# Optimization experiments

Measured on AMD Instinct MI355X. Metric: run time of the kernel, lower is better.

## Reference

```python
import jax, jax.numpy as jnp
import numpy as np

B, S, D, H, HD = 2, 4096, 1024, 16, 64   # batch, seq, hidden, heads, head_dim
BLOCK, W = 64, 8                          # block size, local window in blocks (512 tokens)
ROPE_BASE = 10000.0


def _rope_tables(seq_len, dim, dtype):
    inv_freq = 1.0 / (ROPE_BASE ** (jnp.arange(0, dim, 2, dtype=jnp.float32) / dim))
    t = jnp.arange(seq_len, dtype=jnp.float32)
    freqs = jnp.einsum('i,j->ij', t, inv_freq)          # [S, dim/2]
    emb = jnp.concatenate([freqs, freqs], axis=-1)       # [S, dim]
    return jnp.cos(emb).astype(dtype), jnp.sin(emb).astype(dtype)


def _rotate_half(x):
    x1, x2 = x[..., : x.shape[-1] // 2], x[..., x.shape[-1] // 2:]
    return jnp.concatenate([-x2, x1], axis=-1)


def _apply_rope(q, k, position_ids):
    # q, k: [B, H, S, HD]; position_ids: [B, S]
    cos_t, sin_t = _rope_tables(S, HD, q.dtype)
    cos = cos_t[position_ids][:, None, :, :]             # [B, 1, S, HD]
    sin = sin_t[position_ids][:, None, :, :]
    q_emb = q * cos + _rotate_half(q) * sin
    k_emb = k * cos + _rotate_half(k) * sin
    return q_emb, k_emb


def _block_sparse_attention(q, k, v):
    # Causal block-sparse (sliding window of W blocks), DeepSpeed-style layout.
    # q, k, v: [B, H, S, HD]
    nb = S // BLOCK
    scale = 1.0 / jnp.sqrt(jnp.asarray(HD, q.dtype))
    qb = q.reshape(B, H, nb, BLOCK, HD)
    kb = k.reshape(B, H, nb, BLOCK, HD)
    vb = v.reshape(B, H, nb, BLOCK, HD)
    # block-column indices attended by each block-row: i-W+1 .. i
    idx = jnp.arange(nb)[:, None] - jnp.arange(W - 1, -1, -1)[None, :]   # [nb, W]
    valid = idx >= 0
    idxc = jnp.clip(idx, 0, nb - 1)
    kg = kb[:, :, idxc]                                   # [B, H, nb, W, BLOCK, HD]
    vg = vb[:, :, idxc]
    scores = jnp.einsum('bhnqd,bhnwkd->bhnqwk', qb, kg) * scale  # [B,H,nb,BLOCK,W,BLOCK]
    # absolute positions for causal mask within the window
    qpos = (jnp.arange(nb) * BLOCK)[:, None, None, None] + jnp.arange(BLOCK)[None, :, None, None]  # [nb,BLOCK,1,1]
    kpos = (idxc * BLOCK)[:, None, :, None] + jnp.arange(BLOCK)[None, None, None, :]               # [nb,1,W,BLOCK]
    mask = (kpos <= qpos) & valid[:, None, :, None]       # [nb, BLOCK, W, BLOCK]
    neg = jnp.asarray(-1e9, scores.dtype)
    scores = jnp.where(mask[None, None], scores, neg)
    scores = scores.reshape(B, H, nb, BLOCK, W * BLOCK)
    probs = jax.nn.softmax(scores, axis=-1)
    out = jnp.einsum('bhnqk,bhnkd->bhnqd', probs, vg.reshape(B, H, nb, W * BLOCK, HD))
    return out.reshape(B, H, S, HD)


def setup_inputs() -> dict:
    key = jax.random.key(0)
    ks = jax.random.split(key, 5)
    hidden_states = jax.random.normal(ks[0], (B, S, D), dtype=jnp.float32)
    position_ids = jnp.tile(jnp.arange(S, dtype=jnp.int32)[None, :], (B, 1))
    w_init = lambda k: (jax.random.normal(k, (D, D), dtype=jnp.float32) * 0.02)
    return {
        'hidden_states': hidden_states,
        'position_ids': position_ids,
        'wq': w_init(ks[1]),  # stored [in, out]
        'wk': w_init(ks[2]),
        'wv': w_init(ks[3]),
        'wo': w_init(ks[4]),
    }


def reference(hidden_states, position_ids, wq, wk, wv, wo):
    q = jnp.einsum('bsd,de->bse', hidden_states, wq).reshape(B, S, H, HD).transpose(0, 2, 1, 3)
    k = jnp.einsum('bsd,de->bse', hidden_states, wk).reshape(B, S, H, HD).transpose(0, 2, 1, 3)
    v = jnp.einsum('bsd,de->bse', hidden_states, wv).reshape(B, S, H, HD).transpose(0, 2, 1, 3)
    q, k = _apply_rope(q, k, position_ids)
    attn = _block_sparse_attention(q, k, v)               # [B, H, S, HD]
    attn = attn.transpose(0, 2, 1, 3).reshape(B, S, D)
    return jnp.einsum('bsd,de->bse', attn, wo)
```

## Files before the change

### kernel.cpp

```cpp
#include <hip/hip_runtime.h>
#include <cstdint>
#include <cstddef>

#define B_ 2
#define S_ 4096
#define D_ 1024
#define H_ 16
#define HD_ 64
#define NB_ 64
#define W_ 8
#define M_ (B_*S_)

#define QSCALE 0.18033688011112042f
#define LOG2_10000_OVER_32 0.41524101186092034f

typedef __bf16 bf16_t;
typedef __bf16 bf16x8 __attribute__((ext_vector_type(8)));
typedef float f32x4 __attribute__((ext_vector_type(4)));

#define GLOAD_LDS16(gp, lp) \
  __builtin_amdgcn_global_load_lds((__attribute__((address_space(1))) void*)(gp), \
                                   (__attribute__((address_space(3))) void*)(lp), 16, 0, 0)
#define WAITV(n) asm volatile("s_waitcnt vmcnt(" #n ")" ::: "memory")
#define BAR() do { __builtin_amdgcn_s_barrier(); asm volatile("" ::: "memory"); } while (0)

__global__ __launch_bounds__(256) void prep_kernel(const float* __restrict__ hs,
                                                   bf16_t* __restrict__ hsb,
                                                   const float* __restrict__ w0,
                                                   const float* __restrict__ w1,
                                                   const float* __restrict__ w2,
                                                   const float* __restrict__ w3,
                                                   bf16_t* __restrict__ wT) {
  __shared__ float tile[32][33];
  const int bid = blockIdx.x;
  if (bid < (M_ * D_ / 4) / 256) {
    int i = bid * 256 + threadIdx.x;
    float4 v = ((const float4*)hs)[i];
    union { bf16_t b[4]; uint2 u; } cv;
    cv.b[0] = (bf16_t)v.x; cv.b[1] = (bf16_t)v.y; cv.b[2] = (bf16_t)v.z; cv.b[3] = (bf16_t)v.w;
    ((uint2*)hsb)[i] = cv.u;
  } else {
    const int b2 = bid - (M_ * D_ / 4) / 256;
    const int z = b2 >> 10;
    const int rem = b2 & 1023;
    const int bx = rem & 31, by = rem >> 5;
    const float* w = (z == 0) ? w0 : (z == 1) ? w1 : (z == 2) ? w2 : w3;
    bf16_t* wt = wT + (size_t)z * D_ * D_;
    const int tx = threadIdx.x & 31, ty = threadIdx.x >> 5;
    const int x = bx * 32 + tx;
    const int y0 = by * 32;
    for (int i = ty; i < 32; i += 8)
      tile[i][tx] = w[(size_t)(y0 + i) * D_ + x];
    __syncthreads();
    const int x2 = by * 32 + tx;
    const int y2 = bx * 32;
    for (int i = ty; i < 32; i += 8)
      wt[(size_t)(y2 + i) * D_ + x2] = (bf16_t)tile[tx][i];
  }
}

template<int NBC, int PWN>
__global__ __launch_bounds__(512, 4) void gemm_bk(const bf16_t* __restrict__ A,
                                                  const bf16_t* __restrict__ Bt,
                                                  void* __restrict__ Cbase,
                                                  bf16_t* __restrict__ vt_out,
                                                  const int* __restrict__ pos_ids) {
  constexpr int BN = PWN * 4;
  constexpr int NR = PWN / 32;
  constexpr int BUFEL = 4096 + PWN * 128;
  const int bid = blockIdx.x;
  const int sid = (bid & 7) * (NBC * 8) + (bid >> 3);
  const int mb = sid / NBC, nb = sid % NBC;
  const int mbase = mb * 128, nbase = nb * BN;
  const int tid = threadIdx.x;
  const int wid = tid >> 6, lane = tid & 63;
  const int quad = lane >> 4, l16 = lane & 15;
  const int wr = wid >> 2, wc = wid & 3;

  __shared__ bf16_t lds[3 * BUFEL];

  const int srow = wid * 16 + (lane >> 2);
  const int schunk = (lane & 3) ^ ((lane >> 3) & 3);
  const bf16_t* gAb = A  + (size_t)(mbase + srow) * D_ + schunk * 8;
  const bf16_t* gBb = Bt + (size_t)(nbase + srow) * D_ + schunk * 8;
  const int quadx = (quad ^ ((l16 >> 1) & 3)) * 8;

#define STAGE(kt) do { \
    bf16_t* pa_ = lds + ((kt) % 3) * BUFEL + wid * 512; \
    bf16_t* pb_ = lds + ((kt) % 3) * BUFEL + 4096 + wid * 512; \
    GLOAD_LDS16(gAb + (kt) * 32, pa_); \
    GLOAD_LDS16(gBb + (kt) * 32, pb_); \
    if constexpr (NR == 2) \
      GLOAD_LDS16(gBb + (size_t)128 * D_ + (kt) * 32, pb_ + 4096); } while (0)

#define WTS() do { if constexpr (NR == 2) WAITV(3); else WAITV(2); } while (0)

  f32x4 acc[4][PWN / 16];
#pragma unroll
  for (int m = 0; m < 4; ++m)
#pragma unroll
    for (int n = 0; n < PWN / 16; ++n) acc[m][n] = (f32x4){0.f, 0.f, 0.f, 0.f};

#define PHASE(kt, STG, WT) do { \
    const bf16_t* Ab_ = lds + ((kt) % 3) * BUFEL; \
    const bf16_t* Bb_ = Ab_ + 4096; \
    bf16x8 af_[4], bf_[PWN / 16]; \
    _Pragma("unroll") \
    for (int m = 0; m < 4; ++m) \
      af_[m] = *(const bf16x8*)&Ab_[(wr * 64 + m * 16 + l16) * 32 + quadx]; \
    _Pragma("unroll") \
    for (int n = 0; n < PWN / 16; ++n) \
      bf_[n] = *(const bf16x8*)&Bb_[(wc * PWN + n * 16 + l16) * 32 + quadx]; \
    STG; \
    __builtin_amdgcn_s_setprio(1); \
    _Pragma("unroll") \
    for (int m = 0; m < 4; ++m) \
      _Pragma("unroll") \
      for (int n = 0; n < PWN / 16; ++n) \
        acc[m][n] = __builtin_amdgcn_mfma_f32_16x16x32_bf16(af_[m], bf_[n], acc[m][n], 0, 0, 0); \
    __builtin_amdgcn_s_setprio(0); \
    WT; \
    BAR(); \
  } while (0)

  STAGE(0); STAGE(1);
  WTS();
  BAR();
#pragma unroll 3
  for (int kt = 0; kt < 30; ++kt)
    PHASE(kt, STAGE(kt + 2), WTS());
  PHASE(30, (void)0, WAITV(0));
  PHASE(31, (void)0, (void)0);

  if constexpr (NBC == 12) {
    const int zsl = nb >> 2;
    if (zsl < 2) {
      bf16_t* Cp = (bf16_t*)Cbase + (size_t)zsl * M_ * D_;
      const float qsc = (zsl == 0) ? QSCALE : 1.0f;
      float invf[2];
#pragma unroll
      for (int ni = 0; ni < 2; ++ni)
        invf[ni] = __builtin_exp2f(-(float)(ni * 16 + l16) * LOG2_10000_OVER_32);
      const int colb = (nb & 3) * 256 + wc * 64;
#pragma unroll
      for (int m = 0; m < 4; ++m) {
#pragma unroll
        for (int r = 0; r < 4; ++r) {
          int row = mbase + wr * 64 + m * 16 + quad * 4 + r;
          float fpos = (float)pos_ids[row];
#pragma unroll
          for (int ni = 0; ni < 2; ++ni) {
            float sn, cs;
            __sincosf(fpos * invf[ni], &sn, &cs);
            float x1 = acc[m][ni][r], x2 = acc[m][ni + 2][r];
            int col = colb + ni * 16 + l16;
            Cp[(size_t)row * D_ + col]      = (bf16_t)((x1 * cs - x2 * sn) * qsc);
            Cp[(size_t)row * D_ + col + 32] = (bf16_t)((x2 * cs + x1 * sn) * qsc);
          }
        }
      }
    } else {
      const int h = (nb & 3) * 4 + wc;
      const int g = mb * 2 + wr;
      const int bb = g >> 6, sblk = g & 63;
      size_t vbase = (size_t)(bb * H_ + h) * HD_ * S_;
#pragma unroll
      for (int n = 0; n < 4; ++n) {
        int d = n * 16 + l16;
        union { bf16_t bv[16]; uint4 u[2]; } pk;
#pragma unroll
        for (int r = 0; r < 4; ++r)
#pragma unroll
          for (int mi = 0; mi < 4; ++mi)
            pk.bv[r * 4 + mi] = (bf16_t)acc[mi][n][r];
        size_t addr = vbase + (size_t)d * S_ + (size_t)sblk * 64 + quad * 16;
        *(uint4*)&vt_out[addr]     = pk.u[0];
        *(uint4*)&vt_out[addr + 8] = pk.u[1];
      }
    }
  } else {
    float* Cp = (float*)Cbase;
#pragma unroll
    for (int m = 0; m < 4; ++m)
#pragma unroll
      for (int n = 0; n < PWN / 16; ++n)
#pragma unroll
        for (int r = 0; r < 4; ++r) {
          int row = mbase + wr * 64 + m * 16 + quad * 4 + r;
          int col = nbase + wc * PWN + n * 16 + l16;
          Cp[(size_t)row * D_ + col] = acc[m][n][r];
        }
  }
#undef PHASE
#undef STAGE
#undef WTS
}

__global__ __launch_bounds__(512) void attn_kernel(const bf16_t* __restrict__ q,
                                                   const bf16_t* __restrict__ k,
                                                   const bf16_t* __restrict__ vt,
                                                   bf16_t* __restrict__ o) {
  const int m = blockIdx.x, h = blockIdx.y, b = blockIdx.z;
  const int n0 = m * 2, n1 = n0 + 1;
  const int tid = threadIdx.x;
  const int wid = tid >> 6, lane = tid & 63;
  const int quad = lane >> 4, l16 = lane & 15;
  const int xg = wid >> 2;
  const int wq4 = wid & 3;
  const int nx = n0 + xg;

  __shared__ bf16_t Ks[2][64 * 64];
  __shared__ bf16_t Vs[2][64 * 64];
  __shared__ bf16_t Ps[8][16 * 72];

  const size_t hoff = (size_t)h * HD_;
  const size_t vtbase = (size_t)(b * H_ + h) * HD_ * S_;
  const size_t rowb = (size_t)(b * S_ + nx * 64);

  bf16x8 aq0, aq1;
  {
    const bf16_t* qr = q + (rowb + wq4 * 16 + l16) * D_ + hoff;
    aq0 = *(const bf16x8*)(qr + quad * 8);
    aq1 = *(const bf16x8*)(qr + 32 + quad * 8);
  }

  f32x4 o_acc[4];
  float lsum[4];
#pragma unroll
  for (int t = 0; t < 4; ++t) {
    o_acc[t] = (f32x4){0.f, 0.f, 0.f, 0.f};
    lsum[t] = 0.f;
  }

  const int srK = wid * 8 + (lane >> 3);
  const int scC = ((lane & 7) ^ ((lane >> 3) & 7)) * 8;
  const bf16_t* kbase = k + (size_t)(b * S_) * D_ + hoff;
  const bf16_t* vbase2 = vt + vtbase;
#define STAGE_KV(kb_, buf_) do { \
    GLOAD_LDS16(kbase + (size_t)((kb_) * 64 + srK) * D_ + scC, &Ks[buf_][wid * 512]); \
    GLOAD_LDS16(vbase2 + (size_t)srK * S_ + (kb_) * 64 + scC, &Vs[buf_][wid * 512]); \
  } while (0)

  const int ck0 = (quad ^ (l16 & 7)) * 8;
  const int ck1 = ((quad ^ 4) ^ (l16 & 7)) * 8;

  const int kb0 = (n0 >= W_ - 1) ? n0 - (W_ - 1) : 0;

  STAGE_KV(kb0, kb0 & 1);

  for (int kb = kb0; kb <= n1; ++kb) {
    const int buf = kb & 1;
    if (kb < n1) { STAGE_KV(kb + 1, buf ^ 1); WAITV(2); }
    else        { WAITV(0); }
    BAR();

    const bool active = (xg == 0) ? (kb <= n0) : (kb >= n1 - (W_ - 1));
    if (active) {
      f32x4 sacc[4];
#pragma unroll
      for (int t = 0; t < 4; ++t) sacc[t] = (f32x4){0.f, 0.f, 0.f, 0.f};
#pragma unroll
      for (int t = 0; t < 4; ++t) {
        const int rr = (t * 16 + l16) * 64;
        bf16x8 bk0 = *(const bf16x8*)&Ks[buf][rr + ck0];
        bf16x8 bk1 = *(const bf16x8*)&Ks[buf][rr + ck1];
        sacc[t] = __builtin_amdgcn_mfma_f32_16x16x32_bf16(aq0, bk0, sacc[t], 0, 0, 0);
        sacc[t] = __builtin_amdgcn_mfma_f32_16x16x32_bf16(aq1, bk1, sacc[t], 0, 0, 0);
      }

      const bool diag = (kb == nx);
#pragma unroll
      for (int r = 0; r < 4; ++r) {
        int qpos = wq4 * 16 + quad * 4 + r;
        union { bf16_t bv[4]; uint2 u; } pk;
        float rs = 0.f;
#pragma unroll
        for (int t = 0; t < 4; ++t) {
          float p = __builtin_exp2f(sacc[t][r]);
          if (diag && (t * 16 + l16 > qpos)) p = 0.f;
          rs += p;
          pk.bv[t] = (bf16_t)p;
        }
        lsum[r] += rs;
        *(uint2*)&Ps[wid][(quad * 4 + r) * 72 + l16 * 4] = pk.u;
      }

      bf16x8 pa0 = *(const bf16x8*)&Ps[wid][l16 * 72 + quad * 8];
      bf16x8 pa1 = *(const bf16x8*)&Ps[wid][l16 * 72 + 32 + quad * 8];
#pragma unroll
      for (int t = 0; t < 4; ++t) {
        const int rr = (t * 16 + l16) * 64;
        bf16x8 vb0 = *(const bf16x8*)&Vs[buf][rr + ck0];
        bf16x8 vb1 = *(const bf16x8*)&Vs[buf][rr + ck1];
        o_acc[t] = __builtin_amdgcn_mfma_f32_16x16x32_bf16(pa0, vb0, o_acc[t], 0, 0, 0);
        o_acc[t] = __builtin_amdgcn_mfma_f32_16x16x32_bf16(pa1, vb1, o_acc[t], 0, 0, 0);
      }
    }
    BAR();
  }
#undef STAGE_KV

  float inv[4];
#pragma unroll
  for (int r = 0; r < 4; ++r) {
    float s = lsum[r];
#pragma unroll
    for (int off = 1; off < 16; off <<= 1) s += __shfl_xor(s, off);
    inv[r] = 1.f / s;
  }
#pragma unroll
  for (int t = 0; t < 4; ++t)
#pragma unroll
    for (int r = 0; r < 4; ++r) {
      int row = wq4 * 16 + quad * 4 + r;
      int col = t * 16 + l16;
      o[(rowb + row) * D_ + hoff + col] = (bf16_t)(o_acc[t][r] * inv[r]);
    }
}

extern "C" void kernel_launch(void* const* d_in, const int* in_sizes, int n_in,
                              void* d_out, int out_size, void* d_ws, size_t ws_size,
                              hipStream_t stream) {
  const float* hs = (const float*)d_in[0];
  const int* pos  = (const int*)d_in[1];
  const float* wq = (const float*)d_in[2];
  const float* wk = (const float*)d_in[3];
  const float* wv = (const float*)d_in[4];
  const float* wo = (const float*)d_in[5];

  bf16_t* ws   = (bf16_t*)d_ws;
  bf16_t* hsb  = ws;
  bf16_t* wT   = hsb + (size_t)M_ * D_;
  bf16_t* qkv  = wT + (size_t)4 * D_ * D_;
  bf16_t* attn = qkv + (size_t)3 * M_ * D_;
  bf16_t* qw  = qkv;
  bf16_t* kw  = qkv + (size_t)M_ * D_;
  bf16_t* vtg = qkv + (size_t)2 * M_ * D_;

  prep_kernel<<<dim3((M_ * D_ / 4) / 256 + 4 * 1024), 256, 0, stream>>>(hs, hsb, wq, wk, wv, wo, wT);
  gemm_bk<12, 64><<<dim3(768), dim3(512), 0, stream>>>(hsb, wT, (void*)qkv, vtg, pos);
  attn_kernel<<<dim3(NB_ / 2, H_, B_), 512, 0, stream>>>(qw, kw, vtg, attn);
  gemm_bk<8, 32><<<dim3(512), dim3(512), 0, stream>>>(attn, wT + (size_t)3 * D_ * D_, d_out, nullptr, pos);
}
```

Baseline: 212.1 us.

## Process four query blocks per attention workgroup, two 16-row tiles per wave

Each attention workgroup now covers four consecutive query blocks instead of two. Each wave handles 32 query rows using two MFMA row tiles that share every K/V fragment loaded from LDS. The K/V window staged into shared memory is reused by more query blocks, which cuts global K/V traffic and LDS reads per unit of work. In exchange the grid halves to 512 workgroups, register pressure rises from doubled accumulators, and the Ps buffer doubles in size.

```diff
diff --git a/kernel.cpp b/kernel.cpp
--- a/kernel.cpp
+++ b/kernel.cpp
@@ -201,36 +201,40 @@
                                                    const bf16_t* __restrict__ vt,
                                                    bf16_t* __restrict__ o) {
   const int m = blockIdx.x, h = blockIdx.y, b = blockIdx.z;
-  const int n0 = m * 2, n1 = n0 + 1;
   const int tid = threadIdx.x;
   const int wid = tid >> 6, lane = tid & 63;
   const int quad = lane >> 4, l16 = lane & 15;
-  const int xg = wid >> 2;
-  const int wq4 = wid & 3;
-  const int nx = n0 + xg;
+  const int g = wid >> 1;
+  const int wsub = wid & 1;
+  const int nfirst = m * 4;
+  const int nx = nfirst + g;
+  const int nlast = nfirst + 3;
 
   __shared__ bf16_t Ks[2][64 * 64];
   __shared__ bf16_t Vs[2][64 * 64];
-  __shared__ bf16_t Ps[8][16 * 72];
+  __shared__ bf16_t Ps[8][32 * 72];
 
   const size_t hoff = (size_t)h * HD_;
   const size_t vtbase = (size_t)(b * H_ + h) * HD_ * S_;
   const size_t rowb = (size_t)(b * S_ + nx * 64);
 
-  bf16x8 aq0, aq1;
-  {
-    const bf16_t* qr = q + (rowb + wq4 * 16 + l16) * D_ + hoff;
-    aq0 = *(const bf16x8*)(qr + quad * 8);
-    aq1 = *(const bf16x8*)(qr + 32 + quad * 8);
-  }
-
-  f32x4 o_acc[4];
-  float lsum[4];
-#pragma unroll
-  for (int t = 0; t < 4; ++t) {
-    o_acc[t] = (f32x4){0.f, 0.f, 0.f, 0.f};
-    lsum[t] = 0.f;
-  }
+  bf16x8 aq[2][2];
+#pragma unroll
+  for (int mi = 0; mi < 2; ++mi) {
+    const bf16_t* qr = q + (rowb + wsub * 32 + mi * 16 + l16) * D_ + hoff;
+    aq[mi][0] = *(const bf16x8*)(qr + quad * 8);
+    aq[mi][1] = *(const bf16x8*)(qr + 32 + quad * 8);
+  }
+
+  f32x4 o_acc[2][4];
+  float lsum[2][4];
+#pragma unroll
+  for (int mi = 0; mi < 2; ++mi)
+#pragma unroll
+    for (int t = 0; t < 4; ++t) {
+      o_acc[mi][t] = (f32x4){0.f, 0.f, 0.f, 0.f};
+      lsum[mi][t] = 0.f;
+    }
 
   const int srK = wid * 8 + (lane >> 3);
   const int scC = ((lane & 7) ^ ((lane >> 3) & 7)) * 8;
@@ -244,78 +248,96 @@
   const int ck0 = (quad ^ (l16 & 7)) * 8;
   const int ck1 = ((quad ^ 4) ^ (l16 & 7)) * 8;
 
-  const int kb0 = (n0 >= W_ - 1) ? n0 - (W_ - 1) : 0;
+  const int kb0 = (nfirst >= W_ - 1) ? nfirst - (W_ - 1) : 0;
 
   STAGE_KV(kb0, kb0 & 1);
 
-  for (int kb = kb0; kb <= n1; ++kb) {
+  for (int kb = kb0; kb <= nlast; ++kb) {
     const int buf = kb & 1;
-    if (kb < n1) { STAGE_KV(kb + 1, buf ^ 1); WAITV(2); }
-    else        { WAITV(0); }
+    if (kb < nlast) { STAGE_KV(kb + 1, buf ^ 1); WAITV(2); }
+    else           { WAITV(0); }
     BAR();
 
-    const bool active = (xg == 0) ? (kb <= n0) : (kb >= n1 - (W_ - 1));
+    const bool active = (kb <= nx) && (nx - kb < W_);
     if (active) {
-      f32x4 sacc[4];
-#pragma unroll
-      for (int t = 0; t < 4; ++t) sacc[t] = (f32x4){0.f, 0.f, 0.f, 0.f};
+      const bool diag = (kb == nx);
+      f32x4 sacc[2][4];
+#pragma unroll
+      for (int mi = 0; mi < 2; ++mi)
+#pragma unroll
+        for (int t = 0; t < 4; ++t) sacc[mi][t] = (f32x4){0.f, 0.f, 0.f, 0.f};
 #pragma unroll
       for (int t = 0; t < 4; ++t) {
         const int rr = (t * 16 + l16) * 64;
         bf16x8 bk0 = *(const bf16x8*)&Ks[buf][rr + ck0];
         bf16x8 bk1 = *(const bf16x8*)&Ks[buf][rr + ck1];
-        sacc[t] = __builtin_amdgcn_mfma_f32_16x16x32_bf16(aq0, bk0, sacc[t], 0, 0, 0);
-        sacc[t] = __builtin_amdgcn_mfma_f32_16x16x32_bf16(aq1, bk1, sacc[t], 0, 0, 0);
-      }
-
-      const bool diag = (kb == nx);
-#pragma unroll
-      for (int r = 0; r < 4; ++r) {
-        int qpos = wq4 * 16 + quad * 4 + r;
-        union { bf16_t bv[4]; uint2 u; } pk;
-        float rs = 0.f;
-#pragma unroll
-        for (int t = 0; t < 4; ++t) {
-          float p = __builtin_exp2f(sacc[t][r]);
-          if (diag && (t * 16 + l16 > qpos)) p = 0.f;
-          rs += p;
-          pk.bv[t] = (bf16_t)p;
-        }
-        lsum[r] += rs;
-        *(uint2*)&Ps[wid][(quad * 4 + r) * 72 + l16 * 4] = pk.u;
-      }
-
-      bf16x8 pa0 = *(const bf16x8*)&Ps[wid][l16 * 72 + quad * 8];
-      bf16x8 pa1 = *(const bf16x8*)&Ps[wid][l16 * 72 + 32 + quad * 8];
+#pragma unroll
+        for (int mi = 0; mi < 2; ++mi) {
+          sacc[mi][t] = __builtin_amdgcn_mfma_f32_16x16x32_bf16(aq[mi][0], bk0, sacc[mi][t], 0, 0, 0);
+          sacc[mi][t] = __builtin_amdgcn_mfma_f32_16x16x32_bf16(aq[mi][1], bk1, sacc[mi][t], 0, 0, 0);
+        }
+      }
+
+#pragma unroll
+      for (int mi = 0; mi < 2; ++mi)
+#pragma unroll
+        for (int r = 0; r < 4; ++r) {
+          int qpos = wsub * 32 + mi * 16 + quad * 4 + r;
+          union { bf16_t bv[4]; uint2 u; } pk;
+          float rs = 0.f;
+#pragma unroll
+          for (int t = 0; t < 4; ++t) {
+            float p = __builtin_exp2f(sacc[mi][t][r]);
+            if (diag && (t * 16 + l16 > qpos)) p = 0.f;
+            rs += p;
+            pk.bv[t] = (bf16_t)p;
+          }
+          lsum[mi][r] += rs;
+          *(uint2*)&Ps[wid][(mi * 16 + quad * 4 + r) * 72 + l16 * 4] = pk.u;
+        }
+
+      bf16x8 pa[2][2];
+#pragma unroll
+      for (int mi = 0; mi < 2; ++mi) {
+        pa[mi][0] = *(const bf16x8*)&Ps[wid][(mi * 16 + l16) * 72 + quad * 8];
+        pa[mi][1] = *(const bf16x8*)&Ps[wid][(mi * 16 + l16) * 72 + 32 + quad * 8];
+      }
+
 #pragma unroll
       for (int t = 0; t < 4; ++t) {
         const int rr = (t * 16 + l16) * 64;
         bf16x8 vb0 = *(const bf16x8*)&Vs[buf][rr + ck0];
         bf16x8 vb1 = *(const bf16x8*)&Vs[buf][rr + ck1];
-        o_acc[t] = __builtin_amdgcn_mfma_f32_16x16x32_bf16(pa0, vb0, o_acc[t], 0, 0, 0);
-        o_acc[t] = __builtin_amdgcn_mfma_f32_16x16x32_bf16(pa1, vb1, o_acc[t], 0, 0, 0);
+#pragma unroll
+        for (int mi = 0; mi < 2; ++mi) {
+          o_acc[mi][t] = __builtin_amdgcn_mfma_f32_16x16x32_bf16(pa[mi][0], vb0, o_acc[mi][t], 0, 0, 0);
+          o_acc[mi][t] = __builtin_amdgcn_mfma_f32_16x16x32_bf16(pa[mi][1], vb1, o_acc[mi][t], 0, 0, 0);
+        }
       }
     }
     BAR();
   }
 #undef STAGE_KV
 
-  float inv[4];
-#pragma unroll
-  for (int r = 0; r < 4; ++r) {
-    float s = lsum[r];
-#pragma unroll
-    for (int off = 1; off < 16; off <<= 1) s += __shfl_xor(s, off);
-    inv[r] = 1.f / s;
-  }
-#pragma unroll
-  for (int t = 0; t < 4; ++t)
+#pragma unroll
+  for (int mi = 0; mi < 2; ++mi) {
+    float inv[4];
 #pragma unroll
     for (int r = 0; r < 4; ++r) {
-      int row = wq4 * 16 + quad * 4 + r;
-      int col = t * 16 + l16;
-      o[(rowb + row) * D_ + hoff + col] = (bf16_t)(o_acc[t][r] * inv[r]);
+      float s = lsum[mi][r];
+#pragma unroll
+      for (int off = 1; off < 16; off <<= 1) s += __shfl_xor(s, off);
+      inv[r] = 1.f / s;
     }
+#pragma unroll
+    for (int t = 0; t < 4; ++t)
+#pragma unroll
+      for (int r = 0; r < 4; ++r) {
+        int row = wsub * 32 + mi * 16 + quad * 4 + r;
+        int col = t * 16 + l16;
+        o[(rowb + row) * D_ + hoff + col] = (bf16_t)(o_acc[mi][t][r] * inv[r]);
+      }
+  }
 }
 
 extern "C" void kernel_launch(void* const* d_in, const int* in_sizes, int n_in,
@@ -339,6 +361,6 @@
 
   prep_kernel<<<dim3((M_ * D_ / 4) / 256 + 4 * 1024), 256, 0, stream>>>(hs, hsb, wq, wk, wv, wo, wT);
   gemm_bk<12, 64><<<dim3(768), dim3(512), 0, stream>>>(hsb, wT, (void*)qkv, vtg, pos);
-  attn_kernel<<<dim3(NB_ / 2, H_, B_), 512, 0, stream>>>(qw, kw, vtg, attn);
+  attn_kernel<<<dim3(NB_ / 4, H_, B_), 512, 0, stream>>>(qw, kw, vtg, attn);
   gemm_bk<8, 32><<<dim3(512), dim3(512), 0, stream>>>(attn, wT + (size_t)3 * D_ * D_, d_out, nullptr, pos);
 }
```

Result: slower. 219.8 us (+3.6%).
